# Optimization experiments

Hardware: AMD Instinct MI355X
Metric: run time of the kernel (lower is better)

## Reference

```python
import jax, jax.numpy as jnp
import numpy as np

KERNEL_SIZE = 4
SCALE_FACTOR = 0.5


def setup_inputs() -> dict:
    key = jax.random.key(0)
    k1, k2, k3 = jax.random.split(key, 3)
    batch, in_f, out_f = 4096, 2048, 4096
    x = jax.random.normal(k1, (batch, in_f), dtype=jnp.float32)
    # kaiming-uniform-like scale for weights
    W = jax.random.normal(k2, (out_f, in_f), dtype=jnp.float32) * (1.0 / np.sqrt(in_f))
    b = jax.random.normal(k3, (out_f,), dtype=jnp.float32) * (1.0 / np.sqrt(in_f))
    return {"x": x, "W": W, "b": b}


def reference(x, W, b):
    # Linear: (B, out_f)
    y = jnp.einsum("bi,oi->bo", x, W) + b
    B, out_f = y.shape
    groups = out_f // KERNEL_SIZE
    # MaxPool1d(kernel_size, stride=kernel_size) over feature dim
    pooled = jnp.max(y.reshape(B, groups, KERNEL_SIZE), axis=-1)  # (B, groups)
    # sum over pooled features, then scale -> (B,)
    return jnp.sum(pooled, axis=-1) * SCALE_FACTOR
```

## Files before the change

### kernel.cpp

```cpp
#include <hip/hip_runtime.h>


typedef float  f32x4   __attribute__((ext_vector_type(4)));
typedef short  bf16x8  __attribute__((ext_vector_type(8)));
typedef short  short4v __attribute__((ext_vector_type(4)));

__device__ __forceinline__ short f2bf(float f) {
    union { float f; unsigned u; } v; v.f = f;
    unsigned r = v.u + 0x7FFFu + ((v.u >> 16) & 1u);
    return (short)(r >> 16);
}

__global__ void cvt_kernel(const float* __restrict__ x, const float* __restrict__ w,
                           short* __restrict__ out, long nx, long nw) {
    long total4 = (nx + nw) >> 2;
    long stride = (long)gridDim.x * blockDim.x;
    for (long i = (long)blockIdx.x * blockDim.x + threadIdx.x; i < total4; i += stride) {
        long e = i << 2;
        const float* src = (e < nx) ? (x + e) : (w + (e - nx));
        float4 v = *(const float4*)src;
        short4v s = { f2bf(v.x), f2bf(v.y), f2bf(v.z), f2bf(v.w) };
        *(short4v*)(out + e) = s;
    }
}


#define GLL(gp, ldsp)                                                          \
    __builtin_amdgcn_global_load_lds(                                          \
        (const __attribute__((address_space(1))) unsigned int*)(gp),           \
        (__attribute__((address_space(3))) unsigned int*)(ldsp), 16, 0, 0)

__global__ __launch_bounds__(512, 2) void gemm_pool_kernel(
    const short* __restrict__ X, const short* __restrict__ W,
    const float* __restrict__ bias, float* __restrict__ out, int K)
{
    __shared__ short As[32768];
    __shared__ short Bs[32768];

    const int tid  = threadIdx.x;
    const int lane = tid & 63;
    const int wid  = tid >> 6;
    const int wr   = wid >> 2;
    const int wc   = wid & 3;
    const int hi   = lane >> 4;
    const int lo   = lane & 15;

    const int nwg  = gridDim.x * gridDim.y;
    const int bid  = blockIdx.y * gridDim.x + blockIdx.x;
    const int wgid = (bid & 7) * (nwg >> 3) + (bid >> 3);
    const int brow = (wgid / gridDim.x) * 256;
    const int bcol = (wgid % gridDim.x) * 256;
    const int nk   = K >> 6;

    const int slot0 = hi ^ (lo & 7);
    const int slot1 = (4 + hi) ^ (lo & 7);
    const char* baseA0 = (const char*)As + (((wr * 16 + (lo >> 3)) * 512 + (lo & 7) * 64 + slot0 * 8) << 1);
    const char* baseA1 = (const char*)As + (((wr * 16 + (lo >> 3)) * 512 + (lo & 7) * 64 + slot1 * 8) << 1);
    const char* baseB0 = (const char*)Bs + (((wc * 8  + (lo >> 3)) * 512 + (lo & 7) * 64 + slot0 * 8) << 1);
    const char* baseB1 = (const char*)Bs + (((wc * 8  + (lo >> 3)) * 512 + (lo & 7) * 64 + slot1 * 8) << 1);

    const int idx0 = wid * 2, idx1 = wid * 2 + 1;
    const int cA00 = (idx0 & 7) + ((idx0 >> 3) << 4), cA10 = (idx1 & 7) + ((idx1 >> 3) << 4);
    const int cA01 = cA00 + 8,                         cA11 = cA10 + 8;
    const int cB00 = ((idx0 >> 2) << 3) + (idx0 & 3),  cB10 = ((idx1 >> 2) << 3) + (idx1 & 3);
    const int cB01 = cB00 + 4,                         cB11 = cB10 + 4;
    const int grow = lane >> 3;
    const int gq8  = ((lane & 7) ^ (lane >> 3)) * 8;

    const short* pA00 = X + (size_t)(brow + cA00 * 8 + grow) * K + gq8;
    const short* pA10 = X + (size_t)(brow + cA10 * 8 + grow) * K + gq8;
    const short* pA01 = X + (size_t)(brow + cA01 * 8 + grow) * K + gq8;
    const short* pA11 = X + (size_t)(brow + cA11 * 8 + grow) * K + gq8;
    const short* pB00 = W + (size_t)(bcol + cB00 * 8 + grow) * K + gq8;
    const short* pB10 = W + (size_t)(bcol + cB10 * 8 + grow) * K + gq8;
    const short* pB01 = W + (size_t)(bcol + cB01 * 8 + grow) * K + gq8;
    const short* pB11 = W + (size_t)(bcol + cB11 * 8 + grow) * K + gq8;

    f32x4 acc[8][4] = {};
    bf16x8 a[4][2], b[2][2];

    GLL(pA00, As + cA00 * 512); GLL(pA10, As + cA10 * 512);
    GLL(pB00, Bs + cB00 * 512); GLL(pB10, Bs + cB10 * 512);
    GLL(pB01, Bs + cB01 * 512); GLL(pB11, Bs + cB11 * 512);
    GLL(pA01, As + cA01 * 512); GLL(pA11, As + cA11 * 512);
    GLL(pA00 + 64, As + 16384 + cA00 * 512); GLL(pA10 + 64, As + 16384 + cA10 * 512);
    GLL(pB01 + 64, Bs + 16384 + cB01 * 512); GLL(pB11 + 64, Bs + 16384 + cB11 * 512);
    GLL(pA01 + 64, As + 16384 + cA01 * 512); GLL(pA11 + 64, As + 16384 + cA11 * 512);
    pA00 += 128; pA10 += 128; pA01 += 128; pA11 += 128;
    pB00 += 128; pB10 += 128; pB01 += 128; pB11 += 128;
    asm volatile("s_waitcnt vmcnt(6)" ::: "memory");
    __builtin_amdgcn_s_barrier();

#define TILE_BODY(T, BUF)                                                          \
    {                                                                              \
                   \
        _Pragma("unroll")                                                          \
        for (int mm = 0; mm < 4; ++mm) {                                           \
            a[mm][0] = *(const bf16x8*)(baseA0 + (BUF)*32768 + mm*2048);           \
            a[mm][1] = *(const bf16x8*)(baseA1 + (BUF)*32768 + mm*2048);           \
        }                                                                          \
        _Pragma("unroll")                                                          \
        for (int nn = 0; nn < 2; ++nn) {                                           \
            b[nn][0] = *(const bf16x8*)(baseB0 + (BUF)*32768 + nn*2048);           \
            b[nn][1] = *(const bf16x8*)(baseB1 + (BUF)*32768 + nn*2048);           \
        }                                                                          \
        if ((T) + 1 < nk) {                                                        \
            GLL(pB00 - 64, Bs + (1-(BUF))*16384 + cB00*512);                       \
            GLL(pB10 - 64, Bs + (1-(BUF))*16384 + cB10*512);                       \
        }                                                                          \
        asm volatile("s_waitcnt lgkmcnt(0)" ::: "memory");                         \
        __builtin_amdgcn_s_barrier();                                              \
        __builtin_amdgcn_s_setprio(1);                                             \
        _Pragma("unroll")                                                          \
        for (int mm = 0; mm < 4; ++mm)                                             \
            _Pragma("unroll")                                                      \
            for (int nn = 0; nn < 2; ++nn)                                         \
                _Pragma("unroll")                                                  \
                for (int kk = 0; kk < 2; ++kk)                                     \
                    acc[mm][nn] = __builtin_amdgcn_mfma_f32_16x16x32_bf16(         \
                        a[mm][kk], b[nn][kk], acc[mm][nn], 0, 0, 0);               \
        __builtin_amdgcn_s_setprio(0);                                             \
        __builtin_amdgcn_s_barrier();                                              \
                          \
        _Pragma("unroll")                                                          \
        for (int nn = 0; nn < 2; ++nn) {                                           \
            b[nn][0] = *(const bf16x8*)(baseB0 + (BUF)*32768 + nn*2048 + 4096);    \
            b[nn][1] = *(const bf16x8*)(baseB1 + (BUF)*32768 + nn*2048 + 4096);    \
        }                                                                          \
        if ((T) + 2 < nk) {                                                        \
            GLL(pA00, As + (BUF)*16384 + cA00*512);                                \
            GLL(pA10, As + (BUF)*16384 + cA10*512);                                \
        }                                                                          \
        asm volatile("s_waitcnt lgkmcnt(0)" ::: "memory");                         \
        __builtin_amdgcn_s_barrier();                                              \
        __builtin_amdgcn_s_setprio(1);                                             \
        _Pragma("unroll")                                                          \
        for (int mm = 0; mm < 4; ++mm)                                             \
            _Pragma("unroll")                                                      \
            for (int nn = 0; nn < 2; ++nn)                                         \
                _Pragma("unroll")                                                  \
                for (int kk = 0; kk < 2; ++kk)                                     \
                    acc[mm][2+nn] = __builtin_amdgcn_mfma_f32_16x16x32_bf16(       \
                        a[mm][kk], b[nn][kk], acc[mm][2+nn], 0, 0, 0);             \
        __builtin_amdgcn_s_setprio(0);                                             \
        __builtin_amdgcn_s_barrier();                                              \
                \
        _Pragma("unroll")                                                          \
        for (int mm = 0; mm < 4; ++mm) {                                           \
            a[mm][0] = *(const bf16x8*)(baseA0 + (BUF)*32768 + mm*2048 + 8192);    \
            a[mm][1] = *(const bf16x8*)(baseA1 + (BUF)*32768 + mm*2048 + 8192);    \
        }                                                                          \
        if ((T) + 2 < nk) {                                                        \
            GLL(pB01, Bs + (BUF)*16384 + cB01*512);                                \
            GLL(pB11, Bs + (BUF)*16384 + cB11*512);                                \
        }                                                                          \
        asm volatile("s_waitcnt lgkmcnt(0)" ::: "memory");                         \
        __builtin_amdgcn_s_barrier();                                              \
        __builtin_amdgcn_s_setprio(1);                                             \
        _Pragma("unroll")                                                          \
        for (int mm = 0; mm < 4; ++mm)                                             \
            _Pragma("unroll")                                                      \
            for (int nn = 0; nn < 2; ++nn)                                         \
                _Pragma("unroll")                                                  \
                for (int kk = 0; kk < 2; ++kk)                                     \
                    acc[4+mm][2+nn] = __builtin_amdgcn_mfma_f32_16x16x32_bf16(     \
                        a[mm][kk], b[nn][kk], acc[4+mm][2+nn], 0, 0, 0);           \
        __builtin_amdgcn_s_setprio(0);                                             \
        __builtin_amdgcn_s_barrier();                                              \
                       \
        _Pragma("unroll")                                                          \
        for (int nn = 0; nn < 2; ++nn) {                                           \
            b[nn][0] = *(const bf16x8*)(baseB0 + (BUF)*32768 + nn*2048);           \
            b[nn][1] = *(const bf16x8*)(baseB1 + (BUF)*32768 + nn*2048);           \
        }                                                                          \
        if ((T) + 2 < nk) {                                                        \
            GLL(pA01, As + (BUF)*16384 + cA01*512);                                \
            GLL(pA11, As + (BUF)*16384 + cA11*512);                                \
        }                                                                          \
        asm volatile("s_waitcnt lgkmcnt(0)" ::: "memory");                         \
        __builtin_amdgcn_s_barrier();                                              \
        __builtin_amdgcn_s_setprio(1);                                             \
        _Pragma("unroll")                                                          \
        for (int mm = 0; mm < 4; ++mm)                                             \
            _Pragma("unroll")                                                      \
            for (int nn = 0; nn < 2; ++nn)                                         \
                _Pragma("unroll")                                                  \
                for (int kk = 0; kk < 2; ++kk)                                     \
                    acc[4+mm][nn] = __builtin_amdgcn_mfma_f32_16x16x32_bf16(       \
                        a[mm][kk], b[nn][kk], acc[4+mm][nn], 0, 0, 0);             \
        __builtin_amdgcn_s_setprio(0);                                             \
        if ((T) == nk - 2)      asm volatile("s_waitcnt vmcnt(0)" ::: "memory");   \
        else if ((T) < nk - 2)  asm volatile("s_waitcnt vmcnt(6)" ::: "memory");   \
        __builtin_amdgcn_s_barrier();                                              \
        pA00 += 64; pA10 += 64; pA01 += 64; pA11 += 64;                            \
        pB00 += 64; pB10 += 64; pB01 += 64; pB11 += 64;                            \
    }

    for (int t = 0; t < nk; t += 2) {
        TILE_BODY(t, 0);
        TILE_BODY(t + 1, 1);
    }
#undef TILE_BODY

    float bias_n[4];
#pragma unroll
    for (int nn = 0; nn < 4; ++nn)
        bias_n[nn] = bias[bcol + wc * 64 + nn * 16 + lo];

#pragma unroll
    for (int mm = 0; mm < 8; ++mm) {
#pragma unroll
        for (int j = 0; j < 4; ++j) {
            float part = 0.f;
#pragma unroll
            for (int nn = 0; nn < 4; ++nn) {
                float v = acc[mm][nn][j] + bias_n[nn];
                v = fmaxf(v, __shfl_xor(v, 1));
                v = fmaxf(v, __shfl_xor(v, 2));
                part += v;
            }
            part += __shfl_xor(part, 4);
            part += __shfl_xor(part, 8);
            if (lo == 0)
                atomicAdd(&out[brow + wr * 128 + mm * 16 + hi * 4 + j], part * 0.5f);
        }
    }
}

extern "C" void kernel_launch(void* const* d_in, const int* in_sizes, int n_in,
                              void* d_out, int out_size, void* d_ws, size_t ws_size,
                              hipStream_t stream) {
    const float* x = (const float*)d_in[0];
    const float* W = (const float*)d_in[1];
    const float* b = (const float*)d_in[2];
    float* out = (float*)d_out;

    const int N = in_sizes[2];
    const int K = in_sizes[1] / N;
    const int M = in_sizes[0] / K;

    hipMemsetAsync(out, 0, (size_t)out_size * sizeof(float), stream);

    short* xb = (short*)d_ws;
    short* wb = xb + in_sizes[0];
    cvt_kernel<<<2048, 256, 0, stream>>>(x, W, (short*)d_ws,
                                         (long)in_sizes[0], (long)in_sizes[1]);

    dim3 grid(N / 256, M / 256);
    gemm_pool_kernel<<<grid, 512, 0, stream>>>(xb, wb, b, out, K);
}
```

Before: 95.04 us.

## Fuse fp32-to-bf16 conversion into GEMM loads via register staging

Removes the separate conversion kernel and has the GEMM read fp32 X and W directly. Each thread loads float4 pairs into registers, converts them to bf16, and writes them to LDS, replacing the direct global-to-LDS loads. This drops the extra pass over memory and one kernel launch. The cost is double the global bytes per tile, more VGPR pressure (launch bounds reduced to one block per CU), vmcnt(0) waits that limit load/compute overlap, and conversion ALU work repeated across the 16 block columns and 16 block rows that reread the same data.

After: 140.1 us. +47.4%, slower.

```diff
diff --git a/kernel.cpp b/kernel.cpp
--- a/kernel.cpp
+++ b/kernel.cpp
@@ -3,7 +3,6 @@
 
 typedef float  f32x4   __attribute__((ext_vector_type(4)));
 typedef short  bf16x8  __attribute__((ext_vector_type(8)));
-typedef short  short4v __attribute__((ext_vector_type(4)));
 
 __device__ __forceinline__ short f2bf(float f) {
     union { float f; unsigned u; } v; v.f = f;
@@ -11,27 +10,23 @@
     return (short)(r >> 16);
 }
 
-__global__ void cvt_kernel(const float* __restrict__ x, const float* __restrict__ w,
-                           short* __restrict__ out, long nx, long nw) {
-    long total4 = (nx + nw) >> 2;
-    long stride = (long)gridDim.x * blockDim.x;
-    for (long i = (long)blockIdx.x * blockDim.x + threadIdx.x; i < total4; i += stride) {
-        long e = i << 2;
-        const float* src = (e < nx) ? (x + e) : (w + (e - nx));
-        float4 v = *(const float4*)src;
-        short4v s = { f2bf(v.x), f2bf(v.y), f2bf(v.z), f2bf(v.w) };
-        *(short4v*)(out + e) = s;
-    }
-}
-
-
-#define GLL(gp, ldsp)                                                          \
-    __builtin_amdgcn_global_load_lds(                                          \
-        (const __attribute__((address_space(1))) unsigned int*)(gp),           \
-        (__attribute__((address_space(3))) unsigned int*)(ldsp), 16, 0, 0)
-
-__global__ __launch_bounds__(512, 2) void gemm_pool_kernel(
-    const short* __restrict__ X, const short* __restrict__ W,
+__device__ __forceinline__ bf16x8 cvt8(float4 a, float4 b) {
+    bf16x8 r;
+    r[0] = f2bf(a.x); r[1] = f2bf(a.y); r[2] = f2bf(a.z); r[3] = f2bf(a.w);
+    r[4] = f2bf(b.x); r[5] = f2bf(b.y); r[6] = f2bf(b.z); r[7] = f2bf(b.w);
+    return r;
+}
+
+
+#define STG(P, DST)                                                            \
+    {                                                                          \
+        float4 v0 = *(const float4*)(P);                                       \
+        float4 v1 = *(const float4*)((P) + 4);                                 \
+        *(bf16x8*)(DST) = cvt8(v0, v1);                                        \
+    }
+
+__global__ __launch_bounds__(512, 1) void gemm_pool_kernel(
+    const float* __restrict__ X, const float* __restrict__ W,
     const float* __restrict__ bias, float* __restrict__ out, int K)
 {
     __shared__ short As[32768];
@@ -66,34 +61,40 @@
     const int cB01 = cB00 + 4,                         cB11 = cB10 + 4;
     const int grow = lane >> 3;
     const int gq8  = ((lane & 7) ^ (lane >> 3)) * 8;
-
-    const short* pA00 = X + (size_t)(brow + cA00 * 8 + grow) * K + gq8;
-    const short* pA10 = X + (size_t)(brow + cA10 * 8 + grow) * K + gq8;
-    const short* pA01 = X + (size_t)(brow + cA01 * 8 + grow) * K + gq8;
-    const short* pA11 = X + (size_t)(brow + cA11 * 8 + grow) * K + gq8;
-    const short* pB00 = W + (size_t)(bcol + cB00 * 8 + grow) * K + gq8;
-    const short* pB10 = W + (size_t)(bcol + cB10 * 8 + grow) * K + gq8;
-    const short* pB01 = W + (size_t)(bcol + cB01 * 8 + grow) * K + gq8;
-    const short* pB11 = W + (size_t)(bcol + cB11 * 8 + grow) * K + gq8;
+    short* Awr = As + lane * 8;
+    short* Bwr = Bs + lane * 8;
+
+    const float* pA00 = X + (size_t)(brow + cA00 * 8 + grow) * K + gq8;
+    const float* pA10 = X + (size_t)(brow + cA10 * 8 + grow) * K + gq8;
+    const float* pA01 = X + (size_t)(brow + cA01 * 8 + grow) * K + gq8;
+    const float* pA11 = X + (size_t)(brow + cA11 * 8 + grow) * K + gq8;
+    const float* pB00 = W + (size_t)(bcol + cB00 * 8 + grow) * K + gq8;
+    const float* pB10 = W + (size_t)(bcol + cB10 * 8 + grow) * K + gq8;
+    const float* pB01 = W + (size_t)(bcol + cB01 * 8 + grow) * K + gq8;
+    const float* pB11 = W + (size_t)(bcol + cB11 * 8 + grow) * K + gq8;
 
     f32x4 acc[8][4] = {};
     bf16x8 a[4][2], b[2][2];
-
-    GLL(pA00, As + cA00 * 512); GLL(pA10, As + cA10 * 512);
-    GLL(pB00, Bs + cB00 * 512); GLL(pB10, Bs + cB10 * 512);
-    GLL(pB01, Bs + cB01 * 512); GLL(pB11, Bs + cB11 * 512);
-    GLL(pA01, As + cA01 * 512); GLL(pA11, As + cA11 * 512);
-    GLL(pA00 + 64, As + 16384 + cA00 * 512); GLL(pA10 + 64, As + 16384 + cA10 * 512);
-    GLL(pB01 + 64, Bs + 16384 + cB01 * 512); GLL(pB11 + 64, Bs + 16384 + cB11 * 512);
-    GLL(pA01 + 64, As + 16384 + cA01 * 512); GLL(pA11 + 64, As + 16384 + cA11 * 512);
+    float4 L0, L1, L2, L3;
+
+    STG(pA00, Awr + cA00 * 512); STG(pA10, Awr + cA10 * 512);
+    STG(pB00, Bwr + cB00 * 512); STG(pB10, Bwr + cB10 * 512);
+    STG(pB01, Bwr + cB01 * 512); STG(pB11, Bwr + cB11 * 512);
+    STG(pA01, Awr + cA01 * 512); STG(pA11, Awr + cA11 * 512);
+    STG(pA00 + 64, Awr + 16384 + cA00 * 512); STG(pA10 + 64, Awr + 16384 + cA10 * 512);
+    STG(pB01 + 64, Bwr + 16384 + cB01 * 512); STG(pB11 + 64, Bwr + 16384 + cB11 * 512);
+    STG(pA01 + 64, Awr + 16384 + cA01 * 512); STG(pA11 + 64, Awr + 16384 + cA11 * 512);
+    L0 = *(const float4*)(pB00 + 64); L1 = *(const float4*)(pB00 + 68);
+    L2 = *(const float4*)(pB10 + 64); L3 = *(const float4*)(pB10 + 68);
     pA00 += 128; pA10 += 128; pA01 += 128; pA11 += 128;
     pB00 += 128; pB10 += 128; pB01 += 128; pB11 += 128;
-    asm volatile("s_waitcnt vmcnt(6)" ::: "memory");
+    asm volatile("s_waitcnt lgkmcnt(0)" ::: "memory");
     __builtin_amdgcn_s_barrier();
 
 #define TILE_BODY(T, BUF)                                                          \
     {                                                                              \
-                   \
+                \
+        __builtin_amdgcn_s_barrier();                                              \
         _Pragma("unroll")                                                          \
         for (int mm = 0; mm < 4; ++mm) {                                           \
             a[mm][0] = *(const bf16x8*)(baseA0 + (BUF)*32768 + mm*2048);           \
@@ -104,12 +105,13 @@
             b[nn][0] = *(const bf16x8*)(baseB0 + (BUF)*32768 + nn*2048);           \
             b[nn][1] = *(const bf16x8*)(baseB1 + (BUF)*32768 + nn*2048);           \
         }                                                                          \
+        asm volatile("s_waitcnt vmcnt(0)" ::: "memory");                           \
         if ((T) + 1 < nk) {                                                        \
-            GLL(pB00 - 64, Bs + (1-(BUF))*16384 + cB00*512);                       \
-            GLL(pB10 - 64, Bs + (1-(BUF))*16384 + cB10*512);                       \
-        }                                                                          \
-        asm volatile("s_waitcnt lgkmcnt(0)" ::: "memory");                         \
-        __builtin_amdgcn_s_barrier();                                              \
+            *(bf16x8*)(Bwr + (1-(BUF))*16384 + cB00*512) = cvt8(L0, L1);           \
+            *(bf16x8*)(Bwr + (1-(BUF))*16384 + cB10*512) = cvt8(L2, L3);           \
+        }                                                                          \
+        L0 = *(const float4*)(pA00); L1 = *(const float4*)(pA00 + 4);              \
+        L2 = *(const float4*)(pA10); L3 = *(const float4*)(pA10 + 4);              \
         __builtin_amdgcn_s_setprio(1);                                             \
         _Pragma("unroll")                                                          \
         for (int mm = 0; mm < 4; ++mm)                                             \
@@ -120,19 +122,21 @@
                     acc[mm][nn] = __builtin_amdgcn_mfma_f32_16x16x32_bf16(         \
                         a[mm][kk], b[nn][kk], acc[mm][nn], 0, 0, 0);               \
         __builtin_amdgcn_s_setprio(0);                                             \
-        __builtin_amdgcn_s_barrier();                                              \
-                          \
+        asm volatile("s_waitcnt lgkmcnt(0)" ::: "memory");                         \
+                       \
+        __builtin_amdgcn_s_barrier();                                              \
         _Pragma("unroll")                                                          \
         for (int nn = 0; nn < 2; ++nn) {                                           \
             b[nn][0] = *(const bf16x8*)(baseB0 + (BUF)*32768 + nn*2048 + 4096);    \
             b[nn][1] = *(const bf16x8*)(baseB1 + (BUF)*32768 + nn*2048 + 4096);    \
         }                                                                          \
+        asm volatile("s_waitcnt vmcnt(0)" ::: "memory");                           \
         if ((T) + 2 < nk) {                                                        \
-            GLL(pA00, As + (BUF)*16384 + cA00*512);                                \
-            GLL(pA10, As + (BUF)*16384 + cA10*512);                                \
-        }                                                                          \
-        asm volatile("s_waitcnt lgkmcnt(0)" ::: "memory");                         \
-        __builtin_amdgcn_s_barrier();                                              \
+            *(bf16x8*)(Awr + (BUF)*16384 + cA00*512) = cvt8(L0, L1);               \
+            *(bf16x8*)(Awr + (BUF)*16384 + cA10*512) = cvt8(L2, L3);               \
+        }                                                                          \
+        L0 = *(const float4*)(pB01); L1 = *(const float4*)(pB01 + 4);              \
+        L2 = *(const float4*)(pB11); L3 = *(const float4*)(pB11 + 4);              \
         __builtin_amdgcn_s_setprio(1);                                             \
         _Pragma("unroll")                                                          \
         for (int mm = 0; mm < 4; ++mm)                                             \
@@ -143,19 +147,21 @@
                     acc[mm][2+nn] = __builtin_amdgcn_mfma_f32_16x16x32_bf16(       \
                         a[mm][kk], b[nn][kk], acc[mm][2+nn], 0, 0, 0);             \
         __builtin_amdgcn_s_setprio(0);                                             \
-        __builtin_amdgcn_s_barrier();                                              \
-                \
+        asm volatile("s_waitcnt lgkmcnt(0)" ::: "memory");                         \
+                         \
+        __builtin_amdgcn_s_barrier();                                              \
         _Pragma("unroll")                                                          \
         for (int mm = 0; mm < 4; ++mm) {                                           \
             a[mm][0] = *(const bf16x8*)(baseA0 + (BUF)*32768 + mm*2048 + 8192);    \
             a[mm][1] = *(const bf16x8*)(baseA1 + (BUF)*32768 + mm*2048 + 8192);    \
         }                                                                          \
+        asm volatile("s_waitcnt vmcnt(0)" ::: "memory");                           \
         if ((T) + 2 < nk) {                                                        \
-            GLL(pB01, Bs + (BUF)*16384 + cB01*512);                                \
-            GLL(pB11, Bs + (BUF)*16384 + cB11*512);                                \
-        }                                                                          \
-        asm volatile("s_waitcnt lgkmcnt(0)" ::: "memory");                         \
-        __builtin_amdgcn_s_barrier();                                              \
+            *(bf16x8*)(Bwr + (BUF)*16384 + cB01*512) = cvt8(L0, L1);               \
+            *(bf16x8*)(Bwr + (BUF)*16384 + cB11*512) = cvt8(L2, L3);               \
+        }                                                                          \
+        L0 = *(const float4*)(pA01); L1 = *(const float4*)(pA01 + 4);              \
+        L2 = *(const float4*)(pA11); L3 = *(const float4*)(pA11 + 4);              \
         __builtin_amdgcn_s_setprio(1);                                             \
         _Pragma("unroll")                                                          \
         for (int mm = 0; mm < 4; ++mm)                                             \
@@ -166,19 +172,21 @@
                     acc[4+mm][2+nn] = __builtin_amdgcn_mfma_f32_16x16x32_bf16(     \
                         a[mm][kk], b[nn][kk], acc[4+mm][2+nn], 0, 0, 0);           \
         __builtin_amdgcn_s_setprio(0);                                             \
-        __builtin_amdgcn_s_barrier();                                              \
-                       \
+        asm volatile("s_waitcnt lgkmcnt(0)" ::: "memory");                         \
+                              \
+        __builtin_amdgcn_s_barrier();                                              \
         _Pragma("unroll")                                                          \
         for (int nn = 0; nn < 2; ++nn) {                                           \
             b[nn][0] = *(const bf16x8*)(baseB0 + (BUF)*32768 + nn*2048);           \
             b[nn][1] = *(const bf16x8*)(baseB1 + (BUF)*32768 + nn*2048);           \
         }                                                                          \
+        asm volatile("s_waitcnt vmcnt(0)" ::: "memory");                           \
         if ((T) + 2 < nk) {                                                        \
-            GLL(pA01, As + (BUF)*16384 + cA01*512);                                \
-            GLL(pA11, As + (BUF)*16384 + cA11*512);                                \
-        }                                                                          \
-        asm volatile("s_waitcnt lgkmcnt(0)" ::: "memory");                         \
-        __builtin_amdgcn_s_barrier();                                              \
+            *(bf16x8*)(Awr + (BUF)*16384 + cA01*512) = cvt8(L0, L1);               \
+            *(bf16x8*)(Awr + (BUF)*16384 + cA11*512) = cvt8(L2, L3);               \
+        }                                                                          \
+        L0 = *(const float4*)(pB00); L1 = *(const float4*)(pB00 + 4);              \
+        L2 = *(const float4*)(pB10); L3 = *(const float4*)(pB10 + 4);              \
         __builtin_amdgcn_s_setprio(1);                                             \
         _Pragma("unroll")                                                          \
         for (int mm = 0; mm < 4; ++mm)                                             \
@@ -189,11 +197,11 @@
                     acc[4+mm][nn] = __builtin_amdgcn_mfma_f32_16x16x32_bf16(       \
                         a[mm][kk], b[nn][kk], acc[4+mm][nn], 0, 0, 0);             \
         __builtin_amdgcn_s_setprio(0);                                             \
-        if ((T) == nk - 2)      asm volatile("s_waitcnt vmcnt(0)" ::: "memory");   \
-        else if ((T) < nk - 2)  asm volatile("s_waitcnt vmcnt(6)" ::: "memory");   \
-        __builtin_amdgcn_s_barrier();                                              \
-        pA00 += 64; pA10 += 64; pA01 += 64; pA11 += 64;                            \
-        pB00 += 64; pB10 += 64; pB01 += 64; pB11 += 64;                            \
+        asm volatile("s_waitcnt lgkmcnt(0)" ::: "memory");                         \
+        if ((T) + 3 < nk) {                                                        \
+            pA00 += 64; pA10 += 64; pA01 += 64; pA11 += 64;                        \
+            pB00 += 64; pB10 += 64; pB01 += 64; pB11 += 64;                        \
+        }                                                                          \
     }
 
     for (int t = 0; t < nk; t += 2) {
@@ -241,11 +249,6 @@
 
     hipMemsetAsync(out, 0, (size_t)out_size * sizeof(float), stream);
 
-    short* xb = (short*)d_ws;
-    short* wb = xb + in_sizes[0];
-    cvt_kernel<<<2048, 256, 0, stream>>>(x, W, (short*)d_ws,
-                                         (long)in_sizes[0], (long)in_sizes[1]);
-
     dim3 grid(N / 256, M / 256);
-    gemm_pool_kernel<<<grid, 512, 0, stream>>>(xb, wb, b, out, K);
-}
+    gemm_pool_kernel<<<grid, 512, 0, stream>>>(x, W, b, out, K);
+}
```
